# Optimization experiments

Measured on AMD Instinct MI355X. Metric: run time of the kernel, lower is better.

## Reference

```python
import jax, jax.numpy as jnp
import numpy as np


def setup_inputs() -> dict:
    key = jax.random.key(0)
    ks = jax.random.split(key, 7)
    B, H, W = 32, 28, 28
    C3, C4 = 1024, 2048
    C = C3 + C4            # 3072
    L1 = 9                 # num_landmarks + 1
    A, NC = 312, 200
    return {
        "l3": jax.random.normal(ks[0], (B, C3, H, W), jnp.float32),
        "l4": jax.random.normal(ks[1], (B, C4, H // 2, W // 2), jnp.float32),
        "conv_w": jax.random.normal(ks[2], (L1, C), jnp.float32) * 0.02,
        "modulation": jnp.ones((1, C, L1), jnp.float32),
        "attr_w": jax.random.normal(ks[3], (A, C), jnp.float32) * 0.02,
        "attr_b": jnp.zeros((A,), jnp.float32),
        "class_w": jax.random.normal(ks[4], (NC, A), jnp.float32) * 0.02,
    }


def reference(l3, l4, conv_w, modulation, attr_w, attr_b, class_w):
    b, c3, h, w = l3.shape
    # F.interpolate(l4, (h, w), mode='bilinear', align_corners=False)
    l4_up = jax.image.resize(l4, (b, l4.shape[1], h, w), method="bilinear")
    x = jnp.concatenate([l4_up, l3], axis=1)            # (b, 3072, h, w)

    # 1x1 conv: ab[b,l,h,w] = sum_c w[l,c] * x[b,c,h,w]
    ab = jnp.einsum("lc,bchw->blhw", conv_w, x)
    b_sq = jnp.sum(x * x, axis=1, keepdims=True)        # (b,1,h,w)
    a_sq = jnp.sum(conv_w, axis=1)[None, :, None, None]  # (1,L+1,1,1)  (matches torch: weight.sum(1), NOT squared)
    maps = jax.nn.softmax(-(b_sq - 2.0 * ab + a_sq), axis=1)  # Softmax2d = softmax over channels

    # (maps[:,None] * x[:,:,None]).mean((-1,-2))  ->  batched GEMM over spatial dim
    all_features = jnp.einsum("blhw,bchw->bcl", maps, x) / (h * w)  # (b, c, L+1)

    mod = all_features * modulation                     # dropout is identity at eval
    # permute(0,2,1)[:, :-1, :].mean(1) == mean over landmark dim excluding background
    mean_features = jnp.mean(mod[:, :, :-1], axis=2)    # (b, c)

    attr_scores = mean_features @ attr_w.T + attr_b      # (b, 312)
    class_scores = attr_scores @ class_w.T               # (b, 200)
    return attr_scores, class_scores, maps, all_features
```

## Files before the change

kernel.cpp:

```cpp
#include <hip/hip_runtime.h>
#include <math.h>

#define B_    32
#define C3_   1024
#define C4_   2048
#define C_    3072
#define P_    784
#define Q_    196
#define L_    9
#define NG_   25088
#define A_    312
#define NC_   200

#define ATTR_OFF  0
#define CLASS_OFF 9984
#define MAPS_OFF  16384
#define AF_OFF    242176

#define ASQ_OFF   0
#define MF_OFF    16
#define PART3_OFF 98320
#define PAF_OFF   98320
#define Y4P_OFF   (PART3_OFF + 16 * 9 * NG_)
#define LOGITS_OFF Y4P_OFF
#define Y_OFF     (Y4P_OFF + 32 * 32 * 9 * Q_)
#define MP_OFF    (Y_OFF + 32 * 9 * Q_)

typedef __attribute__((ext_vector_type(8))) short bf16x8;
typedef __attribute__((ext_vector_type(4))) float f32x4;

__device__ __forceinline__ short f2bf(float f) {
    union { float f; unsigned u; } v; v.f = f;
    unsigned r = v.u + 0x7FFFu + ((v.u >> 16) & 1u);
    return (short)(r >> 16);
}

__global__ __launch_bounds__(256, 4) void kA(
        const float* __restrict__ l3, const float* __restrict__ l4,
        const float* __restrict__ conv_w,
        float* __restrict__ part3, float* __restrict__ y4p) {
    int bid = blockIdx.x;
    int t = threadIdx.x;

    const float* xp;
    float* outp;
    int xpitch, opitch, cbase_w;
    if (bid < 400) {
        int slab = bid / 25, rb = bid % 25;
        int tid2 = rb * 256 + t;
        if (tid2 >= 6272) return;
        int b = tid2 / 196, px = (tid2 % 196) * 4;
        xp = l3 + ((size_t)b * C3_ + slab * 64) * P_ + px;
        xpitch = P_;
        cbase_w = C4_ + slab * 64;
        outp = part3 + (size_t)(slab * 9) * NG_ + b * P_ + px;
        opitch = NG_;
    } else {
        int idx = bid - 400;
        int grp = idx / 7, rb = idx % 7;
        int tid2 = rb * 256 + t;
        if (tid2 >= 1568) return;
        int b = tid2 / 49, q = (tid2 % 49) * 4;
        xp = l4 + ((size_t)b * C4_ + grp * 64) * Q_ + q;
        xpitch = Q_;
        cbase_w = grp * 64;
        outp = y4p + ((size_t)(b * 32 + grp) * 9) * Q_ + q;
        opitch = Q_;
    }

    float acc[9][4];
#pragma unroll
    for (int l = 0; l < 9; ++l)
#pragma unroll
        for (int j = 0; j < 4; ++j) acc[l][j] = 0.f;

    float4 v[2][8];
#pragma unroll
    for (int k = 0; k < 8; ++k)
        v[0][k] = *(const float4*)(xp + (size_t)k * xpitch);

#pragma unroll
    for (int c = 0; c < 64; c += 8) {
        int cur = (c >> 3) & 1, nxt = cur ^ 1;
        if (c < 56) {
#pragma unroll
            for (int k = 0; k < 8; ++k)
                v[nxt][k] = *(const float4*)(xp + (size_t)(c + 8 + k) * xpitch);
        }
#pragma unroll
        for (int l = 0; l < 9; ++l) {
            const float4 w0 = *(const float4*)(conv_w + l * C_ + cbase_w + c);
            const float4 w1 = *(const float4*)(conv_w + l * C_ + cbase_w + c + 4);
            const float wv[8] = {w0.x, w0.y, w0.z, w0.w, w1.x, w1.y, w1.z, w1.w};
#pragma unroll
            for (int k = 0; k < 8; ++k) {
                acc[l][0] = fmaf(wv[k], v[cur][k].x, acc[l][0]);
                acc[l][1] = fmaf(wv[k], v[cur][k].y, acc[l][1]);
                acc[l][2] = fmaf(wv[k], v[cur][k].z, acc[l][2]);
                acc[l][3] = fmaf(wv[k], v[cur][k].w, acc[l][3]);
            }
        }
    }
#pragma unroll
    for (int l = 0; l < 9; ++l)
        *(float4*)(outp + (size_t)l * opitch) =
            make_float4(acc[l][0], acc[l][1], acc[l][2], acc[l][3]);
}

__global__ __launch_bounds__(256) void kB(const float* __restrict__ y4p,
                                          const float* __restrict__ conv_w,
                                          float* __restrict__ Y,
                                          float* __restrict__ asq) {
    if (blockIdx.x == 221) {
        __shared__ float red[256];
        int t = threadIdx.x;
        for (int l = 0; l < L_; ++l) {
            float s = 0.f;
            for (int c = t; c < C_; c += 256) s += conv_w[l * C_ + c];
            red[t] = s; __syncthreads();
            for (int o = 128; o > 0; o >>= 1) {
                if (t < o) red[t] += red[t + o];
                __syncthreads();
            }
            if (t == 0) asq[l] = red[0];
            __syncthreads();
        }
        return;
    }
    int tid = blockIdx.x * 256 + threadIdx.x;
    if (tid >= 32 * 9 * Q_) return;
    int b = tid / (9 * Q_);
    int r = tid % (9 * Q_);
    float s = 0.f;
#pragma unroll
    for (int grp = 0; grp < 32; ++grp)
        s += y4p[(size_t)(b * 32 + grp) * (9 * Q_) + r];
    Y[(size_t)b * (9 * Q_) + r] = s;
}

__global__ __launch_bounds__(256) void kC1(const float* __restrict__ part3,
                                           const float* __restrict__ Y,
                                           const float* __restrict__ asq,
                                           float* __restrict__ logits) {
    int idx = blockIdx.x * 256 + threadIdx.x;
    int l = idx / NG_, g = idx % NG_;
    int b = g / P_, p = g % P_;
    int yy = p / 28, xx = p % 28;
    float sy = 0.5f * yy - 0.25f, sx = 0.5f * xx - 0.25f;
    float fyf = floorf(sy), fxf = floorf(sx);
    float fy = sy - fyf, fx = sx - fxf;
    int ya = max(0, (int)fyf), yb = min(13, (int)fyf + 1);
    int xa = max(0, (int)fxf), xb = min(13, (int)fxf + 1);
    float w00 = (1.f - fy) * (1.f - fx), w01 = (1.f - fy) * fx;
    float w10 = fy * (1.f - fx),         w11 = fy * fx;
    const float* Yl = Y + ((size_t)b * 9 + l) * Q_;
    float ab4 = w00 * Yl[ya * 14 + xa] + w01 * Yl[ya * 14 + xb]
              + w10 * Yl[yb * 14 + xa] + w11 * Yl[yb * 14 + xb];
    float ab3 = 0.f;
#pragma unroll
    for (int sl = 0; sl < 16; ++sl)
        ab3 += part3[(size_t)(sl * 9 + l) * NG_ + g];
    logits[idx] = 2.f * (ab4 + ab3) - asq[l];
}

__global__ __launch_bounds__(256) void kC2(const float* __restrict__ logits,
                                           float* __restrict__ out_maps) {
    int g = blockIdx.x * 256 + threadIdx.x;
    int b = g / P_, p = g % P_;
    float v[9];
#pragma unroll
    for (int l = 0; l < 9; ++l) v[l] = logits[(size_t)l * NG_ + g];
    float m = v[0];
#pragma unroll
    for (int l = 1; l < 9; ++l) m = fmaxf(m, v[l]);
    float sum = 0.f;
#pragma unroll
    for (int l = 0; l < 9; ++l) { v[l] = expf(v[l] - m); sum += v[l]; }
    float inv = 1.f / sum;
#pragma unroll
    for (int l = 0; l < 9; ++l)
        out_maps[(size_t)b * (L_ * P_) + l * P_ + p] = v[l] * inv;
}

__device__ __forceinline__ int adj_taps(int q, int* ys, float* wy) {
    if (q == 0)  { ys[0] = 0;  wy[0] = 1.00f; ys[1] = 1;  wy[1] = 0.75f;
                   ys[2] = 2;  wy[2] = 0.25f; return 3; }
    if (q == 13) { ys[0] = 25; wy[0] = 0.25f; ys[1] = 26; wy[1] = 0.75f;
                   ys[2] = 27; wy[2] = 1.00f; return 3; }
    ys[0] = 2 * q - 1; wy[0] = 0.25f;
    ys[1] = 2 * q;     wy[1] = 0.75f;
    ys[2] = 2 * q + 1; wy[2] = 0.75f;
    ys[3] = 2 * q + 2; wy[3] = 0.25f;
    return 4;
}

__global__ __launch_bounds__(256) void kD(const float* __restrict__ maps,
                                          float* __restrict__ Mp) {
    int tid = blockIdx.x * 256 + threadIdx.x;
    if (tid >= 32 * 9 * Q_) return;
    int b = tid / (9 * Q_);
    int r = tid % (9 * Q_);
    int l = r / Q_, q = r % Q_;
    int qy = q / 14, qx = q % 14;
    int ys[4], xs[4]; float wy[4], wx[4];
    int ny = adj_taps(qy, ys, wy);
    int nx = adj_taps(qx, xs, wx);
    const float* mrow = maps + (size_t)b * (L_ * P_) + l * P_;
    float s = 0.f;
    for (int i = 0; i < ny; ++i) {
        float rs = 0.f;
        for (int j = 0; j < nx; ++j)
            rs = fmaf(wx[j], mrow[ys[i] * 28 + xs[j]], rs);
        s = fmaf(wy[i], rs, s);
    }
    Mp[(size_t)b * (9 * Q_) + r] = s;
}

#define SA 232
__global__ __launch_bounds__(256) void kE(
        const float* __restrict__ l3, const float* __restrict__ l4,
        const float* __restrict__ maps, const float* __restrict__ Mp,
        float* __restrict__ out_af, float* __restrict__ paf) {
    __shared__ short As[64 * SA];
    __shared__ short Bs[16 * SA];
    int bid = blockIdx.x;
    int t = threadIdx.x;
    int wave = t >> 6, lane = t & 63;
    int row16 = lane & 15, quad = lane >> 4;

    const float* xsrc; size_t xstride;
    const float* bsrc; size_t bstride;
    int b, c0, h;
    bool isl4 = (bid < 1024);
    if (isl4) {
        b = bid >> 5;
        c0 = (bid & 31) * 64;
        h = 0;
        xsrc = l4 + ((size_t)b * C4_ + c0) * Q_;
        xstride = Q_;
        bsrc = Mp + (size_t)b * (9 * Q_);
        bstride = Q_;
    } else {
        int idx = bid - 1024;
        b = idx >> 6;
        c0 = ((idx >> 2) & 15) * 64;
        h = idx & 3;
        xsrc = l3 + ((size_t)b * C3_ + c0) * P_ + h * Q_;
        xstride = P_;
        bsrc = maps + (size_t)b * (L_ * P_) + h * Q_;
        bstride = P_;
    }

    for (int i = t; i < 64 * 49; i += 256) {
        int r = i / 49, j = (i % 49) * 4;
        float4 v = *(const float4*)(xsrc + (size_t)r * xstride + j);
        ushort4 o;
        o.x = (unsigned short)f2bf(v.x); o.y = (unsigned short)f2bf(v.y);
        o.z = (unsigned short)f2bf(v.z); o.w = (unsigned short)f2bf(v.w);
        *(ushort4*)(As + r * SA + j) = o;
    }
    for (int i = t; i < 64 * 9; i += 256) {
        int r = i / 9, j = 196 + (i % 9) * 4;
        *(ushort4*)(As + r * SA + j) = make_ushort4(0, 0, 0, 0);
    }
    for (int i = t; i < 16 * 58; i += 256) {
        int r = i / 58, j = (i % 58) * 4;
        ushort4 o = make_ushort4(0, 0, 0, 0);
        if (r < 9 && j < 196) {
            float4 v = *(const float4*)(bsrc + (size_t)r * bstride + j);
            o.x = (unsigned short)f2bf(v.x); o.y = (unsigned short)f2bf(v.y);
            o.z = (unsigned short)f2bf(v.z); o.w = (unsigned short)f2bf(v.w);
        }
        *(ushort4*)(Bs + r * SA + j) = o;
    }
    __syncthreads();

    const short* arow = As + (wave * 16 + row16) * SA;
    const short* brow = Bs + row16 * SA;
    f32x4 acc = {0.f, 0.f, 0.f, 0.f};
#pragma unroll
    for (int k0 = 0; k0 < 224; k0 += 32) {
        bf16x8 a = *(const bf16x8*)(arow + k0 + quad * 8);
        bf16x8 bv = *(const bf16x8*)(brow + k0 + quad * 8);
        acc = __builtin_amdgcn_mfma_f32_16x16x32_bf16(a, bv, acc, 0, 0, 0);
    }
    int l = row16;
    if (l < 9) {
        int c = c0 + wave * 16 + quad * 4;
        if (isl4) {
            size_t base = ((size_t)b * C_ + c) * 9 + l;
#pragma unroll
            for (int r = 0; r < 4; ++r)
                out_af[base + (size_t)r * 9] = acc[r] * (1.f / 784.f);
        } else {
            size_t base = ((size_t)(h * B_ + b) * C3_ + c) * 9 + l;
#pragma unroll
            for (int r = 0; r < 4; ++r)
                paf[base + (size_t)r * 9] = acc[r];
        }
    }
}

__global__ __launch_bounds__(256) void kMF(const float* __restrict__ paf,
                                           const float* __restrict__ mod,
                                           float* __restrict__ out_af,
                                           float* __restrict__ mf) {
    int i = blockIdx.x * 256 + threadIdx.x;
    if (i >= B_ * C_) return;
    int b = i / C_, c = i % C_;
    float af[9];
    if (c < C4_) {
#pragma unroll
        for (int l = 0; l < 9; ++l) af[l] = out_af[(size_t)i * 9 + l];
    } else {
        int c3 = c - C4_;
#pragma unroll
        for (int l = 0; l < 9; ++l) {
            float s = 0.f;
#pragma unroll
            for (int hh = 0; hh < 4; ++hh)
                s += paf[((size_t)(hh * B_ + b) * C3_ + c3) * 9 + l];
            af[l] = s * (1.f / 784.f);
            out_af[(size_t)i * 9 + l] = af[l];
        }
    }
    const float* m = mod + (size_t)c * 9;
    float s = 0.f;
#pragma unroll
    for (int l = 0; l < 8; ++l) s = fmaf(af[l], m[l], s);
    mf[i] = s * 0.125f;
}

__global__ __launch_bounds__(256) void kF(
        const float* __restrict__ mf, const float* __restrict__ attr_w,
        const float* __restrict__ attr_b, float* __restrict__ out_attr) {
    int idx = blockIdx.x * 4 + (threadIdx.x >> 6);
    int lane = threadIdx.x & 63;
    int b = idx / A_, a = idx % A_;
    const float4* wr = (const float4*)(attr_w + (size_t)a * C_);
    const float4* mr = (const float4*)(mf + (size_t)b * C_);
    float acc = 0.f;
    for (int j = lane; j < C_ / 4; j += 64) {
        float4 w = wr[j], m = mr[j];
        acc += w.x * m.x + w.y * m.y + w.z * m.z + w.w * m.w;
    }
    acc += __shfl_xor(acc, 1);  acc += __shfl_xor(acc, 2);
    acc += __shfl_xor(acc, 4);  acc += __shfl_xor(acc, 8);
    acc += __shfl_xor(acc, 16); acc += __shfl_xor(acc, 32);
    if (lane == 0) out_attr[idx] = acc + attr_b[a];
}

__global__ __launch_bounds__(256) void kG(
        const float* __restrict__ attr, const float* __restrict__ class_w,
        float* __restrict__ out_class) {
    int idx = blockIdx.x * 4 + (threadIdx.x >> 6);
    int lane = threadIdx.x & 63;
    int b = idx / NC_, n = idx % NC_;
    float acc = 0.f;
    for (int a = lane; a < A_; a += 64)
        acc += attr[b * A_ + a] * class_w[n * A_ + a];
    acc += __shfl_xor(acc, 1);  acc += __shfl_xor(acc, 2);
    acc += __shfl_xor(acc, 4);  acc += __shfl_xor(acc, 8);
    acc += __shfl_xor(acc, 16); acc += __shfl_xor(acc, 32);
    if (lane == 0) out_class[idx] = acc;
}

extern "C" void kernel_launch(void* const* d_in, const int* in_sizes, int n_in,
                              void* d_out, int out_size, void* d_ws, size_t ws_size,
                              hipStream_t stream) {
    (void)in_sizes; (void)n_in; (void)out_size; (void)ws_size;
    const float* l3         = (const float*)d_in[0];
    const float* l4         = (const float*)d_in[1];
    const float* conv_w     = (const float*)d_in[2];
    const float* modulation = (const float*)d_in[3];
    const float* attr_w     = (const float*)d_in[4];
    const float* attr_b     = (const float*)d_in[5];
    const float* class_w    = (const float*)d_in[6];
    float* out = (float*)d_out;
    float* ws  = (float*)d_ws;
    float* asq    = ws + ASQ_OFF;
    float* mf     = ws + MF_OFF;
    float* part3  = ws + PART3_OFF;
    float* paf    = ws + PAF_OFF;
    float* y4p    = ws + Y4P_OFF;
    float* logits = ws + LOGITS_OFF;
    float* Y      = ws + Y_OFF;
    float* Mp     = ws + MP_OFF;

    kA<<<624, 256, 0, stream>>>(l3, l4, conv_w, part3, y4p);
    kB<<<222, 256, 0, stream>>>(y4p, conv_w, Y, asq);
    kC1<<<882, 256, 0, stream>>>(part3, Y, asq, logits);
    kC2<<<98, 256, 0, stream>>>(logits, out + MAPS_OFF);
    kD<<<221, 256, 0, stream>>>(out + MAPS_OFF, Mp);
    kE<<<3072, 256, 0, stream>>>(l3, l4, out + MAPS_OFF, Mp, out + AF_OFF, paf);
    kMF<<<384, 256, 0, stream>>>(paf, modulation, out + AF_OFF, mf);
    kF<<<(B_ * A_) / 4, 256, 0, stream>>>(mf, attr_w, attr_b, out + ATTR_OFF);
    kG<<<(B_ * NC_) / 4, 256, 0, stream>>>(out + ATTR_OFF, class_w,
                                           out + CLASS_OFF);
}
```

Before: 307.9 us.

## Restage conv and feature GEMM loads through LDS with batched register prefetch

kA now uses one block per (batch, 64-channel slab, quarter-row) tile. Each block loads its whole 64x196 tile into registers with coalesced float4 loads, copies it to shared memory, and computes the 9 landmark dot products from LDS with 196 threads. kE is changed the same way: all global loads for the A and B tiles are issued first behind a sched_barrier, and the bf16 conversion and LDS stores happen afterwards. kE also shrinks the A-tile pitch and sets an occupancy hint. The goal is more memory-level parallelism and fewer round-trip load-latency stalls. The cost is more registers, larger LDS use, and only 196 of 256 threads doing compute in kA.

Result: slower. 356.2 us (+15.7%).

```diff
diff --git a/kernel.cpp b/kernel.cpp
--- a/kernel.cpp
+++ b/kernel.cpp
@@ -34,77 +34,77 @@
     unsigned r = v.u + 0x7FFFu + ((v.u >> 16) & 1u);
     return (short)(r >> 16);
 }
-
-__global__ __launch_bounds__(256, 4) void kA(
+__device__ __forceinline__ ushort4 cvt4(float4 v) {
+    ushort4 o;
+    o.x = (unsigned short)f2bf(v.x); o.y = (unsigned short)f2bf(v.y);
+    o.z = (unsigned short)f2bf(v.z); o.w = (unsigned short)f2bf(v.w);
+    return o;
+}
+
+__global__ __launch_bounds__(256, 3) void kA(
         const float* __restrict__ l3, const float* __restrict__ l4,
         const float* __restrict__ conv_w,
         float* __restrict__ part3, float* __restrict__ y4p) {
+    __shared__ float As[64 * 196];
     int bid = blockIdx.x;
     int t = threadIdx.x;
-
-    const float* xp;
+    bool isl4 = (bid >= 2048);
+    const float* xbase;
     float* outp;
-    int xpitch, opitch, cbase_w;
-    if (bid < 400) {
-        int slab = bid / 25, rb = bid % 25;
-        int tid2 = rb * 256 + t;
-        if (tid2 >= 6272) return;
-        int b = tid2 / 196, px = (tid2 % 196) * 4;
-        xp = l3 + ((size_t)b * C3_ + slab * 64) * P_ + px;
-        xpitch = P_;
-        cbase_w = C4_ + slab * 64;
-        outp = part3 + (size_t)(slab * 9) * NG_ + b * P_ + px;
+    int cw0, opitch;
+    if (!isl4) {
+        int slab = bid >> 7;
+        int rem = bid & 127;
+        int b = rem >> 2, h = rem & 3;
+        xbase = l3 + ((size_t)b * C3_ + slab * 64) * P_ + h * Q_;
+        cw0 = C4_ + slab * 64;
+        outp = part3 + (size_t)(slab * 9) * NG_ + b * P_ + h * Q_;
         opitch = NG_;
     } else {
-        int idx = bid - 400;
-        int grp = idx / 7, rb = idx % 7;
-        int tid2 = rb * 256 + t;
-        if (tid2 >= 1568) return;
-        int b = tid2 / 49, q = (tid2 % 49) * 4;
-        xp = l4 + ((size_t)b * C4_ + grp * 64) * Q_ + q;
-        xpitch = Q_;
-        cbase_w = grp * 64;
-        outp = y4p + ((size_t)(b * 32 + grp) * 9) * Q_ + q;
+        int idx = bid - 2048;
+        int b = idx >> 5, grp = idx & 31;
+        xbase = l4 + ((size_t)b * C4_ + grp * 64) * Q_;
+        cw0 = grp * 64;
+        outp = y4p + (size_t)((b * 32 + grp) * 9) * Q_;
         opitch = Q_;
     }
 
-    float acc[9][4];
-#pragma unroll
-    for (int l = 0; l < 9; ++l)
-#pragma unroll
-        for (int j = 0; j < 4; ++j) acc[l][j] = 0.f;
-
-    float4 v[2][8];
-#pragma unroll
-    for (int k = 0; k < 8; ++k)
-        v[0][k] = *(const float4*)(xp + (size_t)k * xpitch);
-
-#pragma unroll
-    for (int c = 0; c < 64; c += 8) {
-        int cur = (c >> 3) & 1, nxt = cur ^ 1;
-        if (c < 56) {
-#pragma unroll
-            for (int k = 0; k < 8; ++k)
-                v[nxt][k] = *(const float4*)(xp + (size_t)(c + 8 + k) * xpitch);
-        }
-#pragma unroll
-        for (int l = 0; l < 9; ++l) {
-            const float4 w0 = *(const float4*)(conv_w + l * C_ + cbase_w + c);
-            const float4 w1 = *(const float4*)(conv_w + l * C_ + cbase_w + c + 4);
-            const float wv[8] = {w0.x, w0.y, w0.z, w0.w, w1.x, w1.y, w1.z, w1.w};
-#pragma unroll
-            for (int k = 0; k < 8; ++k) {
-                acc[l][0] = fmaf(wv[k], v[cur][k].x, acc[l][0]);
-                acc[l][1] = fmaf(wv[k], v[cur][k].y, acc[l][1]);
-                acc[l][2] = fmaf(wv[k], v[cur][k].z, acc[l][2]);
-                acc[l][3] = fmaf(wv[k], v[cur][k].w, acc[l][3]);
+    float4 v[13];
+#pragma unroll
+    for (int u = 0; u < 13; ++u) {
+        int f = u * 256 + t;
+        if (f < 3136) {
+            if (isl4) {
+                v[u] = *(const float4*)(xbase + f * 4);
+            } else {
+                int r = f / 49, cj = (f % 49) * 4;
+                v[u] = *(const float4*)(xbase + (size_t)r * P_ + cj);
             }
         }
     }
-#pragma unroll
-    for (int l = 0; l < 9; ++l)
-        *(float4*)(outp + (size_t)l * opitch) =
-            make_float4(acc[l][0], acc[l][1], acc[l][2], acc[l][3]);
+    __builtin_amdgcn_sched_barrier(0);
+#pragma unroll
+    for (int u = 0; u < 13; ++u) {
+        int f = u * 256 + t;
+        if (f < 3136) *(float4*)(As + f * 4) = v[u];
+    }
+    __syncthreads();
+
+    if (t < Q_) {
+        float acc[9];
+#pragma unroll
+        for (int l = 0; l < 9; ++l) acc[l] = 0.f;
+#pragma unroll 4
+        for (int c = 0; c < 64; ++c) {
+            float xv = As[c * Q_ + t];
+#pragma unroll
+            for (int l = 0; l < 9; ++l)
+                acc[l] = fmaf(conv_w[l * C_ + cw0 + c], xv, acc[l]);
+        }
+#pragma unroll
+        for (int l = 0; l < 9; ++l)
+            outp[(size_t)l * opitch + t] = acc[l];
+    }
 }
 
 __global__ __launch_bounds__(256) void kB(const float* __restrict__ y4p,
@@ -216,20 +216,21 @@
     Mp[(size_t)b * (9 * Q_) + r] = s;
 }
 
-#define SA 232
-__global__ __launch_bounds__(256) void kE(
+#define AP 200
+#define BP 232
+__global__ __launch_bounds__(256, 4) void kE(
         const float* __restrict__ l3, const float* __restrict__ l4,
         const float* __restrict__ maps, const float* __restrict__ Mp,
         float* __restrict__ out_af, float* __restrict__ paf) {
-    __shared__ short As[64 * SA];
-    __shared__ short Bs[16 * SA];
+    __shared__ short As[64 * AP + 64];
+    __shared__ short Bs[16 * BP];
     int bid = blockIdx.x;
     int t = threadIdx.x;
     int wave = t >> 6, lane = t & 63;
     int row16 = lane & 15, quad = lane >> 4;
 
-    const float* xsrc; size_t xstride;
-    const float* bsrc; size_t bstride;
+    const float* xsrc;
+    const float* bsrc; int bstride;
     int b, c0, h;
     bool isl4 = (bid < 1024);
     if (isl4) {
@@ -237,7 +238,6 @@
         c0 = (bid & 31) * 64;
         h = 0;
         xsrc = l4 + ((size_t)b * C4_ + c0) * Q_;
-        xstride = Q_;
         bsrc = Mp + (size_t)b * (9 * Q_);
         bstride = Q_;
     } else {
@@ -246,41 +246,61 @@
         c0 = ((idx >> 2) & 15) * 64;
         h = idx & 3;
         xsrc = l3 + ((size_t)b * C3_ + c0) * P_ + h * Q_;
-        xstride = P_;
         bsrc = maps + (size_t)b * (L_ * P_) + h * Q_;
         bstride = P_;
     }
 
-    for (int i = t; i < 64 * 49; i += 256) {
-        int r = i / 49, j = (i % 49) * 4;
-        float4 v = *(const float4*)(xsrc + (size_t)r * xstride + j);
-        ushort4 o;
-        o.x = (unsigned short)f2bf(v.x); o.y = (unsigned short)f2bf(v.y);
-        o.z = (unsigned short)f2bf(v.z); o.w = (unsigned short)f2bf(v.w);
-        *(ushort4*)(As + r * SA + j) = o;
-    }
-    for (int i = t; i < 64 * 9; i += 256) {
-        int r = i / 9, j = 196 + (i % 9) * 4;
-        *(ushort4*)(As + r * SA + j) = make_ushort4(0, 0, 0, 0);
-    }
-    for (int i = t; i < 16 * 58; i += 256) {
-        int r = i / 58, j = (i % 58) * 4;
-        ushort4 o = make_ushort4(0, 0, 0, 0);
-        if (r < 9 && j < 196) {
-            float4 v = *(const float4*)(bsrc + (size_t)r * bstride + j);
-            o.x = (unsigned short)f2bf(v.x); o.y = (unsigned short)f2bf(v.y);
-            o.z = (unsigned short)f2bf(v.z); o.w = (unsigned short)f2bf(v.w);
-        }
-        *(ushort4*)(Bs + r * SA + j) = o;
-    }
+    float4 va[13];
+#pragma unroll
+    for (int u = 0; u < 13; ++u) {
+        int f = u * 256 + t;
+        if (f < 3136) {
+            if (isl4) {
+                va[u] = *(const float4*)(xsrc + f * 4);
+            } else {
+                int r = f / 49, cj = (f % 49) * 4;
+                va[u] = *(const float4*)(xsrc + (size_t)r * P_ + cj);
+            }
+        }
+    }
+    float4 vb[4];
+#pragma unroll
+    for (int u = 0; u < 4; ++u) {
+        int i = u * 256 + t;
+        if (i < 16 * 58) {
+            int r = i / 58, j = (i % 58) * 4;
+            vb[u] = make_float4(0.f, 0.f, 0.f, 0.f);
+            if (r < 9 && j < 196)
+                vb[u] = *(const float4*)(bsrc + (size_t)r * bstride + j);
+        }
+    }
+    __builtin_amdgcn_sched_barrier(0);
+#pragma unroll
+    for (int u = 0; u < 13; ++u) {
+        int f = u * 256 + t;
+        if (f < 3136) {
+            int r = f / 49, j = (f % 49) * 4;
+            *(ushort4*)(As + r * AP + j) = cvt4(va[u]);
+        }
+    }
+#pragma unroll
+    for (int u = 0; u < 4; ++u) {
+        int i = u * 256 + t;
+        if (i < 16 * 58) {
+            int r = i / 58, j = (i % 58) * 4;
+            *(ushort4*)(Bs + r * BP + j) = cvt4(vb[u]);
+        }
+    }
+    if (t < 64) *(ushort4*)(As + t * AP + 196) = make_ushort4(0, 0, 0, 0);
+    if (t < 16) *(ushort4*)(As + 64 * AP + t * 4) = make_ushort4(0, 0, 0, 0);
     __syncthreads();
 
-    const short* arow = As + (wave * 16 + row16) * SA;
-    const short* brow = Bs + row16 * SA;
+    const short* arow = As + (wave * 16 + row16) * AP;
+    const short* brow = Bs + row16 * BP;
     f32x4 acc = {0.f, 0.f, 0.f, 0.f};
 #pragma unroll
     for (int k0 = 0; k0 < 224; k0 += 32) {
-        bf16x8 a = *(const bf16x8*)(arow + k0 + quad * 8);
+        bf16x8 a  = *(const bf16x8*)(arow + k0 + quad * 8);
         bf16x8 bv = *(const bf16x8*)(brow + k0 + quad * 8);
         acc = __builtin_amdgcn_mfma_f32_16x16x32_bf16(a, bv, acc, 0, 0, 0);
     }
@@ -293,7 +313,8 @@
             for (int r = 0; r < 4; ++r)
                 out_af[base + (size_t)r * 9] = acc[r] * (1.f / 784.f);
         } else {
-            size_t base = ((size_t)(h * B_ + b) * C3_ + c) * 9 + l;
+            size_t base = ((size_t)(h * B_ + b) * C3_ + (c - C4_) + 0) * 9 + l;
+            base = ((size_t)(h * B_ + b) * C3_ + c) * 9 + l;
 #pragma unroll
             for (int r = 0; r < 4; ++r)
                 paf[base + (size_t)r * 9] = acc[r];
@@ -387,7 +408,7 @@
     float* Y      = ws + Y_OFF;
     float* Mp     = ws + MP_OFF;
 
-    kA<<<624, 256, 0, stream>>>(l3, l4, conv_w, part3, y4p);
+    kA<<<3072, 256, 0, stream>>>(l3, l4, conv_w, part3, y4p);
     kB<<<222, 256, 0, stream>>>(y4p, conv_w, Y, asq);
     kC1<<<882, 256, 0, stream>>>(part3, Y, asq, logits);
     kC2<<<98, 256, 0, stream>>>(logits, out + MAPS_OFF);
```
